# Optimization experiments

Measured on AMD Instinct MI355X. Metric: run time of the kernel, lower is better.

## Reference

```python
import jax, jax.numpy as jnp
import numpy as np

# --- static configuration (from init_kwargs / chosen original_size) ---
IMG = 1024            # PromptGetter image_size
DS = 64               # PromptGetter downsizing
ORIG_H, ORIG_W = 1080, 1920
SCALE = IMG / max(ORIG_H, ORIG_W)                 # ResizeLongestSide scale
PRE_H = int(np.floor(ORIG_H * SCALE + 0.5))       # get_prepadded_size -> 576
PRE_W = int(np.floor(ORIG_W * SCALE + 0.5))       # -> 1024
NW = int(ORIG_W * SCALE) // DS                    # grid columns (n_w)
NUM_GRIDS = (IMG // DS) ** 2                      # safe upper bound on grid ids (256)
DEFAULT_THR_TARGET = 0.65
NUM_BG = 1
NUM_LABELS = 16


def setup_inputs() -> dict:
    key = jax.random.key(0)
    k1, k2 = jax.random.split(key)
    return {
        "image_embeddings": jax.random.normal(k1, (1, 256, 64, 64), dtype=jnp.float32),
        "reference_feats": jax.random.normal(k2, (NUM_LABELS, 1, 256), dtype=jnp.float32),
        "original_size": jnp.array([ORIG_H, ORIG_W], dtype=jnp.int32),
        "threshold": jnp.zeros((1, 1), dtype=jnp.float32),  # 0 -> default_threshold_target
        "num_bg_points": 1,
    }


def _postprocess(sim):
    """SAM postprocess_masks: 64x64 -> IMGxIMG -> crop prepadded -> original size."""
    m = jax.image.resize(sim, (IMG, IMG), method="linear")  # align_corners=False bilinear
    m = m[:PRE_H, :PRE_W]
    return jax.image.resize(m, (ORIG_H, ORIG_W), method="linear")


def _point_selection(mask_sim, thr):
    h, w = mask_sim.shape
    flat = mask_sim.reshape(-1)

    # background: k lowest-similarity points (topk largest=False)
    _, bg_idx = jax.lax.top_k(-flat, NUM_BG)
    bg_row = bg_idx // w
    bg_col = bg_idx - bg_row * w
    bg_coords = jnp.stack([bg_col, bg_row], axis=-1).astype(jnp.float32)  # (NUM_BG, 2) as (x, y)

    # foreground: per-grid-cell best-scoring point above threshold.
    # The original gathers torch.where(mask_sim > thr) points and picks the max
    # score per downsized grid cell; here we keep fixed shapes by masking and
    # doing a segment-max over all pixels (same selected points/scores).
    idx = jnp.arange(h * w)
    ys = idx // w
    xs = idx % w
    valid = flat > thr
    grid = ((jnp.floor(ys * SCALE / DS)) * NW + jnp.floor(xs * SCALE / DS)).astype(jnp.int32)
    score = jnp.where(valid, flat, -jnp.inf)
    best = jax.ops.segment_max(score, grid, num_segments=NUM_GRIDS)
    is_best = valid & (flat == best[grid])
    cand = jnp.where(is_best, idx, h * w)
    best_idx = jax.ops.segment_min(cand, grid, num_segments=NUM_GRIDS)  # first max, like torch.topk(k=1)
    grid_ok = jnp.isfinite(best) & (best_idx < h * w)
    safe_idx = jnp.minimum(best_idx, h * w - 1)
    bx = jnp.where(grid_ok, (safe_idx % w).astype(jnp.float32), 0.0)
    by = jnp.where(grid_ok, (safe_idx // w).astype(jnp.float32), 0.0)
    sc = jnp.where(grid_ok, best, -jnp.inf)
    pts = jnp.stack([bx, by, sc], axis=-1)  # (NUM_GRIDS, 3) = (x, y, score)

    # sort by score, descending (empty grid cells sink to the end with -inf)
    order = jnp.argsort(-pts[:, -1])
    return pts[order], bg_coords


def reference(image_embeddings, reference_feats, original_size, threshold, num_bg_points):
    tf = image_embeddings[0]                                   # (C, H, W)
    tf = tf / jnp.linalg.norm(tf, axis=0, keepdims=True)       # channelwise L2 normalize
    c = tf.shape[0]
    tf = tf.reshape(c, -1)                                     # (C, HW)
    thr = ((threshold == 0).astype(threshold.dtype) * DEFAULT_THR_TARGET + threshold)[0, 0]

    def per_label(ref_feat):                                   # ref_feat (1, C)
        sim = (ref_feat @ tf).reshape(64, 64)                  # cosine sim map
        return _point_selection(_postprocess(sim), thr)

    points_scores, bg_coords = jax.vmap(per_label)(reference_feats)
    return points_scores, bg_coords
```

## Files before the change

### kernel.cpp

```cpp
#include <hip/hip_runtime.h>
#include <cmath>
#include <climits>

#define NLAB 16
#define GRIDS 144
#define HOUT 1080
#define WOUT 1920
#define KS2 0.53333336f
#define KS1 0.0625f
#define NEG_MARK -1.0e30f
#define POS_BIG   1.0e30f

__device__ __forceinline__ void taps64(int i, int& t0, int& t1, float& g) {
    float s = ((float)i + 0.5f) * KS1 - 0.5f;
    float f = floorf(s);
    g = s - f;
    int j = (int)f;
    t0 = j < 0 ? 0 : j;
    t1 = j + 1; if (t1 > 63) t1 = 63;
}

__device__ __forceinline__ void fused_taps(int P, int n1m1, int& base,
                                           float& w0, float& w1, float& w2) {
    float sx = ((float)P + 0.5f) * KS2 - 0.5f;
    float fx = floorf(sx);
    float bx = sx - fx;
    int tx = (int)fx;
    int i0 = tx < 0 ? 0 : tx;
    int i1 = tx + 1; if (i1 > n1m1) i1 = n1m1;
    int a0, a1; float ga; taps64(i0, a0, a1, ga);
    int b0, b1; float gb; taps64(i1, b0, b1, gb);
    base = a0;
    w0 = (1.f - bx) * (1.f - ga); w1 = 0.f; w2 = 0.f;
    float c1 = (1.f - bx) * ga;
    if (a1 == base) w0 += c1; else w1 += c1;
    float c2 = bx * (1.f - gb);
    { int o = b0 - base; if (o == 0) w0 += c2; else if (o == 1) w1 += c2; else w2 += c2; }
    float c3 = bx * gb;
    { int o = b1 - base; if (o == 0) w0 += c3; else if (o == 1) w1 += c3; else w2 += c3; }
}

__launch_bounds__(256)
__global__ void sim_kernel(const float* __restrict__ emb,
                           const float* __restrict__ ref,
                           float* __restrict__ sim) {
    __shared__ float rlds[NLAB * 256];
    __shared__ float red[16][NLAB][16];
    __shared__ float n2red[16][16];
    int tid = threadIdx.x;
    for (int i = tid; i < NLAB * 256; i += 256) rlds[i] = ref[i];
    __syncthreads();
    int posl = tid & 15;
    int chunk = tid >> 4;
    int p = blockIdx.x * 16 + posl;
    float acc[NLAB];
#pragma unroll
    for (int l = 0; l < NLAB; ++l) acc[l] = 0.f;
    float n2 = 0.f;
    int cbase = chunk * 16;
#pragma unroll
    for (int cc = 0; cc < 16; ++cc) {
        int c = cbase + cc;
        float v = emb[c * 4096 + p];
        n2 = fmaf(v, v, n2);
#pragma unroll
        for (int l = 0; l < NLAB; ++l)
            acc[l] = fmaf(rlds[l * 256 + c], v, acc[l]);
    }
#pragma unroll
    for (int l = 0; l < NLAB; ++l) red[posl][l][chunk] = acc[l];
    n2red[posl][chunk] = n2;
    __syncthreads();
    int l = chunk;
    float dot = 0.f, nn = 0.f;
#pragma unroll
    for (int k = 0; k < 16; ++k) { dot += red[posl][l][k]; nn += n2red[posl][k]; }
    sim[l * 4096 + p] = dot / sqrtf(nn);
}

__launch_bounds__(256)
__global__ void eval_kernel(const float* __restrict__ simAll,
                            const float* __restrict__ thrPtr,
                            float* __restrict__ gVal, int* __restrict__ gIdx,
                            float* __restrict__ mVal, int* __restrict__ mIdx) {
    int label = blockIdx.x / GRIDS;
    int g = blockIdx.x - label * GRIDS;
    int gy = g >> 4, gx = g & 15;
    int tid = threadIdx.x;

    __shared__ float s8[8][9];
    __shared__ float4 wxT[120];
    __shared__ float4 wyT[120];
    __shared__ int   boundsS[6];
    __shared__ float rv[4], rmv[4];
    __shared__ int   ri[4], rmi[4];

    int X0 = gx * 120, Y0 = gy * 120;
    int r0, c0; float dw0, dw1, dw2;
    fused_taps(Y0, 575, r0, dw0, dw1, dw2);
    fused_taps(X0, 1023, c0, dw0, dw1, dw2);

    if (tid < 6) boundsS[tid] = (tid == 0) ? 0 : 120;
    if (tid < 64) {
        int j = tid >> 3, k = tid & 7;
        int rr = r0 + j; if (rr > 63) rr = 63;
        int kk = c0 + k; if (kk > 63) kk = 63;
        s8[j][k] = simAll[label * 4096 + rr * 64 + kk];
    }
    int my_rbl = -1;
    if (tid < 120) {
        int kb; float w0, w1, w2;
        fused_taps(X0 + tid, 1023, kb, w0, w1, w2);
        wxT[tid] = make_float4(w0, w1, w2, __int_as_float(kb - c0));
    } else if (tid >= 128 && tid < 248) {
        int r = tid - 128;
        int rb; float w0, w1, w2;
        fused_taps(Y0 + r, 575, rb, w0, w1, w2);
        my_rbl = rb - r0;
        wyT[r] = make_float4(w0, w1, w2, __int_as_float(my_rbl));
    }
    __syncthreads();

    if (tid >= 129 && tid < 248) {
        int r = tid - 128;
        int prev = __float_as_int(wyT[r - 1].w);
        if (my_rbl != prev) boundsS[my_rbl] = r;
    }

    float t0v = thrPtr[0];
    float thr = (t0v == 0.0f) ? 0.65f : t0v;

    float C0 = 0.f, C1 = 0.f, C2 = 0.f, C3 = 0.f, C4 = 0.f, C5 = 0.f, C6 = 0.f;
    int c = 0, h = 0;
    if (tid < 240) {
        h = (tid >= 120) ? 1 : 0;
        c = tid - h * 120;
        float4 wx = wxT[c];
        int kb = __float_as_int(wx.w);
#define COLSUM(J) fmaf(wx.z, s8[J][kb + 2], fmaf(wx.y, s8[J][kb + 1], wx.x * s8[J][kb]))
        C0 = COLSUM(0); C1 = COLSUM(1); C2 = COLSUM(2); C3 = COLSUM(3);
        C4 = COLSUM(4); C5 = COLSUM(5); C6 = COLSUM(6);
#undef COLSUM
    }
    __syncthreads();

    int b5 = 120;
    int b4 = boundsS[4] < b5 ? boundsS[4] : b5;
    int b3 = boundsS[3] < b4 ? boundsS[3] : b4;
    int b2 = boundsS[2] < b3 ? boundsS[2] : b3;
    int b1 = boundsS[1] < b2 ? boundsS[1] : b2;
    int b0 = 0;

    float bmax = NEG_MARK; int bidx = INT_MAX;
    float vmin = POS_BIG;  int vidx = INT_MAX;

    if (tid < 240) {
        int ybase = h * 60, yend = ybase + 60;
#define PHASE(LO, HI, CA, CB, CC)                                            \
        {   int lo = (LO) > ybase ? (LO) : ybase;                            \
            int hi = (HI) < yend ? (HI) : yend;                              \
            int idx = (Y0 + lo) * WOUT + X0 + c;                             \
            _Pragma("unroll 4")                                              \
            for (int r = lo; r < hi; ++r) {                                  \
                float4 wy = wyT[r];                                          \
                float val = fmaf(wy.z, CC, fmaf(wy.y, CB, wy.x * CA));       \
                if (val > bmax) { bmax = val; bidx = idx; }                  \
                if (val < vmin) { vmin = val; vidx = idx; }                  \
                idx += WOUT;                                                 \
            } }
        PHASE(b0, b1, C0, C1, C2)
        PHASE(b1, b2, C1, C2, C3)
        PHASE(b2, b3, C2, C3, C4)
        PHASE(b3, b4, C3, C4, C5)
        PHASE(b4, b5, C4, C5, C6)
#undef PHASE
    }

    for (int off = 32; off; off >>= 1) {
        float ov = __shfl_xor(bmax, off); int oi = __shfl_xor(bidx, off);
        if (ov > bmax || (ov == bmax && oi < bidx)) { bmax = ov; bidx = oi; }
        float mv2 = __shfl_xor(vmin, off); int mi2 = __shfl_xor(vidx, off);
        if (mv2 < vmin || (mv2 == vmin && mi2 < vidx)) { vmin = mv2; vidx = mi2; }
    }
    int wave = tid >> 6;
    if ((tid & 63) == 0) { rv[wave] = bmax; ri[wave] = bidx; rmv[wave] = vmin; rmi[wave] = vidx; }
    __syncthreads();
    if (tid == 0) {
#pragma unroll
        for (int w = 1; w < 4; ++w) {
            float ov = rv[w]; int oi = ri[w];
            if (ov > rv[0] || (ov == rv[0] && oi < ri[0])) { rv[0] = ov; ri[0] = oi; }
            float mv2 = rmv[w]; int mi2 = rmi[w];
            if (mv2 < rmv[0] || (mv2 == rmv[0] && mi2 < rmi[0])) { rmv[0] = mv2; rmi[0] = mi2; }
        }
        int o = label * GRIDS + g;
        if (rv[0] > thr) { gVal[o] = rv[0]; gIdx[o] = ri[0]; }
        else             { gVal[o] = NEG_MARK; gIdx[o] = INT_MAX; }
        mVal[o] = rmv[0]; mIdx[o] = rmi[0];
    }
}

__launch_bounds__(256)
__global__ void final_kernel(const float* __restrict__ gVal, const int* __restrict__ gIdx,
                             const float* __restrict__ mVal, const int* __restrict__ mIdx,
                             float* __restrict__ out) {
    int l = blockIdx.x;
    int tid = threadIdx.x;
    __shared__ float sc[256]; __shared__ int sg[256];
    __shared__ float lx[256], ly[256];

    float score = NEG_MARK;
    float x = 0.0f, y = 0.0f;
    if (tid < GRIDS) {
        float v = gVal[l * GRIDS + tid];
        int i = gIdx[l * GRIDS + tid];
        if (v != NEG_MARK && i < HOUT * WOUT) {
            score = v;
            x = (float)(i % WOUT);
            y = (float)(i / WOUT);
        }
    }
    sc[tid] = score; sg[tid] = tid; lx[tid] = x; ly[tid] = y;
    __syncthreads();

    for (int k = 2; k <= 256; k <<= 1) {
        for (int j = k >> 1; j > 0; j >>= 1) {
            int i2 = tid ^ j;
            if (i2 > tid) {
                float s_a = sc[tid], s_b = sc[i2];
                int g_a = sg[tid], g_b = sg[i2];
                bool up = ((tid & k) == 0);
                bool b_before_a = (s_b > s_a) || (s_b == s_a && g_b < g_a);
                if (b_before_a == up) {
                    sc[tid] = s_b; sc[i2] = s_a;
                    sg[tid] = g_b; sg[i2] = g_a;
                }
            }
            __syncthreads();
        }
    }

    int g2 = sg[tid];
    float* o = out + (l * 256 + tid) * 3;
    o[0] = lx[g2]; o[1] = ly[g2]; o[2] = sc[tid];

    __shared__ float mv[256]; __shared__ int mi[256];
    float v2 = POS_BIG; int i3 = INT_MAX;
    if (tid < GRIDS) { v2 = mVal[l * GRIDS + tid]; i3 = mIdx[l * GRIDS + tid]; }
    mv[tid] = v2; mi[tid] = i3;
    __syncthreads();
    for (int s2 = 128; s2 > 0; s2 >>= 1) {
        if (tid < s2) {
            float ov = mv[tid + s2]; int oi = mi[tid + s2];
            if (ov < mv[tid] || (ov == mv[tid] && oi < mi[tid])) { mv[tid] = ov; mi[tid] = oi; }
        }
        __syncthreads();
    }
    if (tid == 0) {
        int bi = mi[0];
        out[NLAB * 256 * 3 + l * 2 + 0] = (float)(bi % WOUT);
        out[NLAB * 256 * 3 + l * 2 + 1] = (float)(bi / WOUT);
    }
}

extern "C" void kernel_launch(void* const* d_in, const int* in_sizes, int n_in,
                              void* d_out, int out_size, void* d_ws, size_t ws_size,
                              hipStream_t stream) {
    const float* emb = (const float*)d_in[0];
    const float* ref = (const float*)d_in[1];
    const float* thr = (const float*)d_in[3];
    float* out = (float*)d_out;

    float* sim  = (float*)d_ws;
    float* gVal = sim + NLAB * 4096;
    int*   gIdx = (int*)(gVal + NLAB * GRIDS);
    float* mVal = (float*)(gIdx + NLAB * GRIDS);
    int*   mIdx = (int*)(mVal + NLAB * GRIDS);

    sim_kernel<<<256, 256, 0, stream>>>(emb, ref, sim);
    eval_kernel<<<NLAB * GRIDS, 256, 0, stream>>>(sim, thr, gVal, gIdx, mVal, mIdx);
    final_kernel<<<NLAB, 256, 0, stream>>>(gVal, gIdx, mVal, mIdx, out);
}
```

Before: 92.65 us.

## Fuse cosine-similarity computation into per-grid eval kernel, recomputing 8x8 sim patch

Removes the separate sim_kernel and its global sim buffer. Each eval block now loads the 8x8 spatial patch of all 256 embedding channels it needs, computes the normalized dot product with its label's reference feature in LDS, and builds its s8 tile from that. This saves a kernel launch and the global round trip. In exchange it recomputes overlapping patches across 2304 blocks, adds an extra 16KB of LDS per block, and adds per-block load and compute work.

```diff
diff --git a/kernel.cpp b/kernel.cpp
--- a/kernel.cpp
+++ b/kernel.cpp
@@ -41,53 +41,19 @@
 }
 
 __launch_bounds__(256)
-__global__ void sim_kernel(const float* __restrict__ emb,
-                           const float* __restrict__ ref,
-                           float* __restrict__ sim) {
-    __shared__ float rlds[NLAB * 256];
-    __shared__ float red[16][NLAB][16];
-    __shared__ float n2red[16][16];
-    int tid = threadIdx.x;
-    for (int i = tid; i < NLAB * 256; i += 256) rlds[i] = ref[i];
-    __syncthreads();
-    int posl = tid & 15;
-    int chunk = tid >> 4;
-    int p = blockIdx.x * 16 + posl;
-    float acc[NLAB];
-#pragma unroll
-    for (int l = 0; l < NLAB; ++l) acc[l] = 0.f;
-    float n2 = 0.f;
-    int cbase = chunk * 16;
-#pragma unroll
-    for (int cc = 0; cc < 16; ++cc) {
-        int c = cbase + cc;
-        float v = emb[c * 4096 + p];
-        n2 = fmaf(v, v, n2);
-#pragma unroll
-        for (int l = 0; l < NLAB; ++l)
-            acc[l] = fmaf(rlds[l * 256 + c], v, acc[l]);
-    }
-#pragma unroll
-    for (int l = 0; l < NLAB; ++l) red[posl][l][chunk] = acc[l];
-    n2red[posl][chunk] = n2;
-    __syncthreads();
-    int l = chunk;
-    float dot = 0.f, nn = 0.f;
-#pragma unroll
-    for (int k = 0; k < 16; ++k) { dot += red[posl][l][k]; nn += n2red[posl][k]; }
-    sim[l * 4096 + p] = dot / sqrtf(nn);
-}
-
-__launch_bounds__(256)
-__global__ void eval_kernel(const float* __restrict__ simAll,
-                            const float* __restrict__ thrPtr,
-                            float* __restrict__ gVal, int* __restrict__ gIdx,
-                            float* __restrict__ mVal, int* __restrict__ mIdx) {
+__global__ void simeval_kernel(const float* __restrict__ emb,
+                               const float* __restrict__ ref,
+                               const float* __restrict__ thrPtr,
+                               float* __restrict__ gVal, int* __restrict__ gIdx,
+                               float* __restrict__ mVal, int* __restrict__ mIdx) {
     int label = blockIdx.x / GRIDS;
     int g = blockIdx.x - label * GRIDS;
     int gy = g >> 4, gx = g & 15;
     int tid = threadIdx.x;
 
+    __shared__ float el[64 * 65];
+    __shared__ float rldsS[256];
+    __shared__ float s8full[64];
     __shared__ float s8[8][9];
     __shared__ float4 wxT[120];
     __shared__ float4 wyT[120];
@@ -99,13 +65,51 @@
     int r0, c0; float dw0, dw1, dw2;
     fused_taps(Y0, 575, r0, dw0, dw1, dw2);
     fused_taps(X0, 1023, c0, dw0, dw1, dw2);
-
+    int rbase = r0 > 56 ? 56 : r0;
+    int cbase = c0 > 56 ? 56 : c0;
+    int ro = r0 - rbase, co = c0 - cbase;
+
+    rldsS[tid] = ref[label * 256 + tid];
     if (tid < 6) boundsS[tid] = (tid == 0) ? 0 : 120;
+
+    int c_l = tid >> 2;
+    int jj = (tid & 3) * 2;
+    int pos = tid >> 2;
+    int q = tid & 3;
+    float dot = 0.f, n2 = 0.f;
+    for (int cc = 0; cc < 4; ++cc) {
+        const float* src = emb + (cc * 64 + c_l) * 4096 + (rbase + jj) * 64 + cbase;
+        float a0 = src[0], a1 = src[1], a2 = src[2], a3 = src[3];
+        float a4 = src[4], a5 = src[5], a6 = src[6], a7 = src[7];
+        float b0 = src[64], b1 = src[65], b2 = src[66], b3 = src[67];
+        float b4 = src[68], b5 = src[69], b6 = src[70], b7 = src[71];
+        __syncthreads();
+        float* d0 = &el[c_l * 65 + jj * 8];
+        d0[0] = a0; d0[1] = a1; d0[2] = a2; d0[3] = a3;
+        d0[4] = a4; d0[5] = a5; d0[6] = a6; d0[7] = a7;
+        float* d1 = &el[c_l * 65 + (jj + 1) * 8];
+        d1[0] = b0; d1[1] = b1; d1[2] = b2; d1[3] = b3;
+        d1[4] = b4; d1[5] = b5; d1[6] = b6; d1[7] = b7;
+        __syncthreads();
+        int cb = cc * 64 + q * 16;
+#pragma unroll
+        for (int s = 0; s < 16; ++s) {
+            float v = el[(q * 16 + s) * 65 + pos];
+            float rr = rldsS[cb + s];
+            dot = fmaf(rr, v, dot);
+            n2 = fmaf(v, v, n2);
+        }
+    }
+    dot += __shfl_xor(dot, 1); dot += __shfl_xor(dot, 2);
+    n2  += __shfl_xor(n2, 1);  n2  += __shfl_xor(n2, 2);
+    if (q == 0) s8full[pos] = dot / sqrtf(n2);
+    __syncthreads();
+
     if (tid < 64) {
         int j = tid >> 3, k = tid & 7;
-        int rr = r0 + j; if (rr > 63) rr = 63;
-        int kk = c0 + k; if (kk > 63) kk = 63;
-        s8[j][k] = simAll[label * 4096 + rr * 64 + kk];
+        int js = j + ro; if (js > 7) js = 7;
+        int ks = k + co; if (ks > 7) ks = 7;
+        s8[j][k] = s8full[js * 8 + ks];
     }
     int my_rbl = -1;
     if (tid < 120) {
@@ -271,13 +275,11 @@
     const float* thr = (const float*)d_in[3];
     float* out = (float*)d_out;
 
-    float* sim  = (float*)d_ws;
-    float* gVal = sim + NLAB * 4096;
+    float* gVal = (float*)d_ws;
     int*   gIdx = (int*)(gVal + NLAB * GRIDS);
     float* mVal = (float*)(gIdx + NLAB * GRIDS);
     int*   mIdx = (int*)(mVal + NLAB * GRIDS);
 
-    sim_kernel<<<256, 256, 0, stream>>>(emb, ref, sim);
-    eval_kernel<<<NLAB * GRIDS, 256, 0, stream>>>(sim, thr, gVal, gIdx, mVal, mIdx);
+    simeval_kernel<<<NLAB * GRIDS, 256, 0, stream>>>(emb, ref, thr, gVal, gIdx, mVal, mIdx);
     final_kernel<<<NLAB, 256, 0, stream>>>(gVal, gIdx, mVal, mIdx, out);
 }
```

Measured after the change: 116.0 us. 25.2% more time.
